# Performance work log

Measured on AMD Instinct MI355X. Metric: run time of the kernel, lower is better.

The kernel has to match this reference:

```python
import jax, jax.numpy as jnp
import numpy as np

B, n, D, L, Hff, heads = 64, 512, 128, 3, 512, 8
N = B * n
deg = 16
E = N * deg
dh = D // heads
EPS = 1e-5


def setup_inputs() -> dict:
    key = jax.random.key(0)
    ks = jax.random.split(key, 16)
    x = jax.random.normal(ks[0], (N, D), jnp.float32)
    # within-graph random edges (TSP kNN-style), offset per graph
    src = jax.random.randint(ks[1], (B, n * deg), 0, n)
    dst = jax.random.randint(ks[2], (B, n * deg), 0, n)
    off = (jnp.arange(B) * n)[:, None]
    edge_index = jnp.stack([(src + off).reshape(-1), (dst + off).reshape(-1)]).astype(jnp.int32)
    edge_attr = jax.random.normal(ks[3], (E, D), jnp.float32)
    batch = jnp.repeat(jnp.arange(B, dtype=jnp.int32), n)
    s = 0.02
    wk = jax.random.split(ks[4], 8)
    w = lambda k, shape: jax.random.normal(k, shape, jnp.float32) * s
    return dict(
        x=x, edge_index=edge_index, edge_attr=edge_attr, batch=batch,
        Wq=w(wk[0], (L, D, D)), bq=jnp.zeros((L, D), jnp.float32),
        Wk=w(wk[1], (L, D, D)), bk=jnp.zeros((L, D), jnp.float32),
        Wv=w(wk[2], (L, D, D)), bv=jnp.zeros((L, D), jnp.float32),
        We=w(wk[3], (L, D, D)),  # lin_edge has no bias in PyG TransformerConv
        Wskip=w(wk[4], (L, D, D)), bskip=jnp.zeros((L, D), jnp.float32),
        gn_g=jnp.ones((L - 1, D), jnp.float32), gn_b=jnp.zeros((L - 1, D), jnp.float32),
        gn_a=jnp.ones((L - 1, D), jnp.float32),
        ffW1=w(wk[5], (D, Hff)), ffb1=jnp.zeros((Hff,), jnp.float32),
        fgn_g=jnp.ones((Hff,), jnp.float32), fgn_b=jnp.zeros((Hff,), jnp.float32),
        fgn_a=jnp.ones((Hff,), jnp.float32),
        ffW2=w(wk[6], (Hff, D)), ffb2=jnp.zeros((D,), jnp.float32),
    )


def _graph_norm(x, batch, gamma, beta, alpha):
    # GraphNorm: per-graph mean/var per channel, learnable mean scale alpha
    mean = jax.ops.segment_sum(x, batch, num_segments=B) / n
    xc = x - alpha * mean[batch]
    var = jax.ops.segment_sum(xc * xc, batch, num_segments=B) / n
    return gamma * xc * jax.lax.rsqrt(var[batch] + EPS) + beta


def _transformer_conv(x, src, dst, ea, Wq, bq, Wk, bk, Wv, bv, We, Ws, bs):
    q = (x @ Wq + bq).reshape(-1, heads, dh)
    k = (x @ Wk + bk).reshape(-1, heads, dh)
    v = (x @ Wv + bv).reshape(-1, heads, dh)
    e = (ea @ We).reshape(-1, heads, dh)
    ke = k[src] + e                                   # [E, h, dh]
    score = jnp.einsum('ehd,ehd->eh', q[dst], ke) / np.sqrt(dh)
    m = jax.ops.segment_max(score, dst, num_segments=N)
    ex = jnp.exp(score - m[dst])
    denom = jax.ops.segment_sum(ex, dst, num_segments=N)
    alpha = ex / denom[dst]                           # softmax over in-neighbors
    msg = alpha[..., None] * (v[src] + e)
    out = jax.ops.segment_sum(msg, dst, num_segments=N).reshape(-1, D)
    return out + x @ Ws + bs                          # root/skip connection


def reference(x, edge_index, edge_attr, batch, Wq, bq, Wk, bk, Wv, bv, We, Wskip, bskip,
              gn_g, gn_b, gn_a, ffW1, ffb1, fgn_g, fgn_b, fgn_a, ffW2, ffb2):
    src, dst = edge_index[0], edge_index[1]
    for i in range(L):
        x = _transformer_conv(x, src, dst, edge_attr, Wq[i], bq[i], Wk[i], bk[i],
                              Wv[i], bv[i], We[i], Wskip[i], bskip[i])
        if i < L - 1:
            x = _graph_norm(jax.nn.gelu(x, approximate=False), batch, gn_g[i], gn_b[i], gn_a[i])
        else:
            h = jax.nn.gelu(x @ ffW1 + ffb1, approximate=False)
            h = _graph_norm(h, batch, fgn_g, fgn_b, fgn_a)
            x = h @ ffW2 + ffb2
    node_embeddings = x.reshape(B, n, D)
    graph_feat = jax.ops.segment_sum(x, batch, num_segments=B) / n  # mean pool
    return node_embeddings, graph_feat
```

## Files before the change

### kernel.cpp

```cpp
#include <hip/hip_runtime.h>
#include <hip/hip_bf16.h>
#include <math.h>

typedef unsigned short u16;
typedef __attribute__((ext_vector_type(4))) float floatx4;
typedef __attribute__((ext_vector_type(8))) short shortx8;

#define NB 64
#define NNODE 512
#define NTOT (NB*NNODE)
#define DDIM 128
#define DEG 16
#define NEDGE (NTOT*DEG)
#define HFF 512
#define EPSV 1e-5f
#define BFRAG_U16 16384
#define EPI_LD 136

__device__ __forceinline__ float bf2f(u16 u){
  union { unsigned int i; float f; } v; v.i = ((unsigned int)u) << 16; return v.f;
}
__device__ __forceinline__ u16 f2bf(float f){
  union { float f; unsigned int i; } v; v.f = f;
  unsigned int r = v.i + 0x7FFFu + ((v.i >> 16) & 1u);
  return (u16)(r >> 16);
}
__device__ __forceinline__ float gelu_f(float x){
  return 0.5f * x * (1.0f + erff(x * 0.70710678118654752f));
}

__global__ void prep_kernel(const float* __restrict__ x, u16* __restrict__ xb,
                            int* __restrict__ counts, float* __restrict__ pool){
  int gid = blockIdx.x*256 + threadIdx.x;
  if (gid < NTOT) counts[gid] = 0;
  if (gid < NB*DDIM) pool[gid] = 0.f;
  int i = gid*4;
  float4 f = *(const float4*)(x + i);
  ushort4 o; o.x = f2bf(f.x); o.y = f2bf(f.y); o.z = f2bf(f.z); o.w = f2bf(f.w);
  *(ushort4*)(xb + i) = o;
}

__global__ void hist_kernel(const int* __restrict__ dst, int* __restrict__ counts){
  int e = blockIdx.x*256 + threadIdx.x; atomicAdd(&counts[dst[e]], 1);
}
__global__ void scan_kernel(const int* counts, int* row_ptr, int* cursor){
  __shared__ int part[1024];
  int t = threadIdx.x; int base = t*32;
  int loc[32]; int s = 0;
  #pragma unroll
  for (int i = 0; i < 32; ++i){ loc[i] = counts[base+i]; s += loc[i]; }
  part[t] = s; __syncthreads();
  for (int off = 1; off < 1024; off <<= 1){
    int v = (t >= off) ? part[t-off] : 0;
    __syncthreads(); part[t] += v; __syncthreads();
  }
  int run = part[t] - s;
  #pragma unroll
  for (int i = 0; i < 32; ++i){ row_ptr[base+i] = run; cursor[base+i] = run; run += loc[i]; }
  if (t == 0) row_ptr[NTOT] = part[1023];
}
__global__ void scatter_kernel(const int* __restrict__ src, const int* __restrict__ dst,
                               int* __restrict__ cursor, int* __restrict__ ssrc, int* __restrict__ seid){
  int e = blockIdx.x*256 + threadIdx.x;
  int d = dst[e];
  int pos = atomicAdd(&cursor[d], 1);
  ssrc[pos] = src[e]; seid[pos] = e;
}

__global__ __launch_bounds__(512, 2)
void egemm3_kernel(const float* __restrict__ ea, const int* __restrict__ seid,
                   const float* __restrict__ We, u16* __restrict__ eout, int niter){
  __shared__ u16 bfrag[3*BFRAG_U16];
  __shared__ u16 epi_s[8*16*EPI_LD];
  const int t = threadIdx.x;
  const int wave = t >> 6, lane = t & 63, quad = lane >> 4, l16 = lane & 15;
  for (int p = wave; p < 12; p += 8){
    const int l = p >> 2, kk = p & 3;
    const float* Bp = We + (size_t)l*DDIM*DDIM;
    #pragma unroll
    for (int nt = 0; nt < 8; ++nt){
      int colB = nt*16 + l16;
      shortx8 pk;
      #pragma unroll
      for (int j = 0; j < 8; ++j)
        pk[j] = (short)f2bf(Bp[(size_t)(kk*32 + quad*8 + j)*DDIM + colB]);
      *(shortx8*)&bfrag[((size_t)l*2048 + (kk*8 + nt)*64 + lane)*8] = pk;
    }
  }
  __syncthreads();
  u16* epi = &epi_s[wave*16*EPI_LD];
  float4 pf[16];
  int it = blockIdx.x;
  if (it < niter){
    const int w0 = it*256 + wave*32;
    const long br0 = (long)seid[w0 + l16], br1 = (long)seid[w0 + 16 + l16];
    #pragma unroll
    for (int kk = 0; kk < 4; ++kk){
      pf[kk*4+0] = *(const float4*)(ea + br0*DDIM + kk*32 + quad*8);
      pf[kk*4+1] = *(const float4*)(ea + br0*DDIM + kk*32 + quad*8 + 4);
      pf[kk*4+2] = *(const float4*)(ea + br1*DDIM + kk*32 + quad*8);
      pf[kk*4+3] = *(const float4*)(ea + br1*DDIM + kk*32 + quad*8 + 4);
    }
  }
  while (it < niter){
    const int wrow0 = it*256 + wave*32;
    const int nxt = it + gridDim.x;
    shortx8 af[2][4];
    #pragma unroll
    for (int kk = 0; kk < 4; ++kk){
      float4 x0 = pf[kk*4+0], x1 = pf[kk*4+1], y0 = pf[kk*4+2], y1 = pf[kk*4+3];
      shortx8 a0, a1;
      a0[0]=(short)f2bf(x0.x); a0[1]=(short)f2bf(x0.y); a0[2]=(short)f2bf(x0.z); a0[3]=(short)f2bf(x0.w);
      a0[4]=(short)f2bf(x1.x); a0[5]=(short)f2bf(x1.y); a0[6]=(short)f2bf(x1.z); a0[7]=(short)f2bf(x1.w);
      a1[0]=(short)f2bf(y0.x); a1[1]=(short)f2bf(y0.y); a1[2]=(short)f2bf(y0.z); a1[3]=(short)f2bf(y0.w);
      a1[4]=(short)f2bf(y1.x); a1[5]=(short)f2bf(y1.y); a1[6]=(short)f2bf(y1.z); a1[7]=(short)f2bf(y1.w);
      af[0][kk] = a0; af[1][kk] = a1;
    }
    if (nxt < niter){
      const int w2 = nxt*256 + wave*32;
      const long br0 = (long)seid[w2 + l16], br1 = (long)seid[w2 + 16 + l16];
      #pragma unroll
      for (int kk = 0; kk < 4; ++kk){
        pf[kk*4+0] = *(const float4*)(ea + br0*DDIM + kk*32 + quad*8);
        pf[kk*4+1] = *(const float4*)(ea + br0*DDIM + kk*32 + quad*8 + 4);
        pf[kk*4+2] = *(const float4*)(ea + br1*DDIM + kk*32 + quad*8);
        pf[kk*4+3] = *(const float4*)(ea + br1*DDIM + kk*32 + quad*8 + 4);
      }
    }
    #pragma unroll
    for (int l = 0; l < 3; ++l){
      floatx4 acc[2][8] = {};
      #pragma unroll
      for (int kk = 0; kk < 4; ++kk){
        #pragma unroll
        for (int nt = 0; nt < 8; ++nt){
          shortx8 bfr = *(const shortx8*)&bfrag[((size_t)l*2048 + (kk*8 + nt)*64 + lane)*8];
          acc[0][nt] = __builtin_amdgcn_mfma_f32_16x16x32_bf16(af[0][kk], bfr, acc[0][nt], 0, 0, 0);
          acc[1][nt] = __builtin_amdgcn_mfma_f32_16x16x32_bf16(af[1][kk], bfr, acc[1][nt], 0, 0, 0);
        }
      }
      u16* o16 = eout + (size_t)l*NEDGE*DDIM;
      #pragma unroll
      for (int mt = 0; mt < 2; ++mt){
        #pragma unroll
        for (int nt = 0; nt < 8; ++nt){
          #pragma unroll
          for (int r = 0; r < 4; ++r)
            epi[(quad*4 + r)*EPI_LD + nt*16 + l16] = f2bf(acc[mt][nt][r]);
        }
        #pragma unroll
        for (int j = 0; j < 4; ++j){
          int row = j*4 + quad;
          uint4 d = *(const uint4*)&epi[row*EPI_LD + l16*8];
          *(uint4*)(o16 + (size_t)(wrow0 + mt*16 + row)*DDIM + l16*8) = d;
        }
      }
    }
    it = nxt;
  }
}

struct Gemm2Cfg {
  const float* B[4];
  const float* bias[4];
  float* o32[4];
  u16* o16[4];
  const float* nA;
  const float* nBp;
  int ldb, ld_out, bcolmul, ocolmul, gelu, mtiles;
};

template<bool AFF>
__global__ __launch_bounds__(256, 3)
void gemm2_kernel(const u16* __restrict__ Ab, Gemm2Cfg cfg){
  __shared__ u16 lds[BFRAG_U16 + 4*16*EPI_LD];
  const int t = threadIdx.x;
  const int wave = t >> 6, lane = t & 63, quad = lane >> 4, l16 = lane & 15;
  const int cb = blockIdx.y;
  const float* Bp = cfg.B[cb];
  const int col0b = cb * cfg.bcolmul;
  {
    const int kk = wave;
    #pragma unroll
    for (int nt = 0; nt < 8; ++nt){
      int colB = col0b + nt*16 + l16;
      shortx8 pk;
      #pragma unroll
      for (int j = 0; j < 8; ++j)
        pk[j] = (short)f2bf(Bp[(size_t)(kk*32 + quad*8 + j)*cfg.ldb + colB]);
      *(shortx8*)&lds[((kk*8 + nt)*64 + lane)*8] = pk;
    }
  }
  __syncthreads();
  const float* biasp = cfg.bias[cb];
  const int col0o = cb * cfg.ocolmul;
  float bias_r[8];
  #pragma unroll
  for (int nt = 0; nt < 8; ++nt)
    bias_r[nt] = biasp ? biasp[col0o + nt*16 + l16] : 0.0f;
  u16* epi = &lds[BFRAG_U16 + wave*16*EPI_LD];

  for (int tile = blockIdx.x; tile < cfg.mtiles; tile += gridDim.x){
    const int wrow0 = tile*128 + wave*32;
    const int r0 = wrow0 + l16, r1 = r0 + 16;
    const int g = wrow0 >> 9;
    shortx8 af[2][4];
    #pragma unroll
    for (int kk = 0; kk < 4; ++kk){
      shortx8 a0 = *(const shortx8*)(Ab + (size_t)r0*128 + kk*32 + quad*8);
      shortx8 a1 = *(const shortx8*)(Ab + (size_t)r1*128 + kk*32 + quad*8);
      if (AFF){
        const float4 A0 = *(const float4*)(cfg.nA  + (size_t)g*DDIM + kk*32 + quad*8);
        const float4 A1 = *(const float4*)(cfg.nA  + (size_t)g*DDIM + kk*32 + quad*8 + 4);
        const float4 B0 = *(const float4*)(cfg.nBp + (size_t)g*DDIM + kk*32 + quad*8);
        const float4 B1 = *(const float4*)(cfg.nBp + (size_t)g*DDIM + kk*32 + quad*8 + 4);
        u16* p0 = (u16*)&a0; u16* p1 = (u16*)&a1;
        p0[0]=f2bf(bf2f(p0[0])*A0.x+B0.x); p0[1]=f2bf(bf2f(p0[1])*A0.y+B0.y);
        p0[2]=f2bf(bf2f(p0[2])*A0.z+B0.z); p0[3]=f2bf(bf2f(p0[3])*A0.w+B0.w);
        p0[4]=f2bf(bf2f(p0[4])*A1.x+B1.x); p0[5]=f2bf(bf2f(p0[5])*A1.y+B1.y);
        p0[6]=f2bf(bf2f(p0[6])*A1.z+B1.z); p0[7]=f2bf(bf2f(p0[7])*A1.w+B1.w);
        p1[0]=f2bf(bf2f(p1[0])*A0.x+B0.x); p1[1]=f2bf(bf2f(p1[1])*A0.y+B0.y);
        p1[2]=f2bf(bf2f(p1[2])*A0.z+B0.z); p1[3]=f2bf(bf2f(p1[3])*A0.w+B0.w);
        p1[4]=f2bf(bf2f(p1[4])*A1.x+B1.x); p1[5]=f2bf(bf2f(p1[5])*A1.y+B1.y);
        p1[6]=f2bf(bf2f(p1[6])*A1.z+B1.z); p1[7]=f2bf(bf2f(p1[7])*A1.w+B1.w);
      }
      af[0][kk] = a0; af[1][kk] = a1;
    }
    floatx4 acc[2][8] = {};
    #pragma unroll
    for (int kk = 0; kk < 4; ++kk){
      #pragma unroll
      for (int nt = 0; nt < 8; ++nt){
        shortx8 bfr = *(const shortx8*)&lds[((kk*8 + nt)*64 + lane)*8];
        acc[0][nt] = __builtin_amdgcn_mfma_f32_16x16x32_bf16(af[0][kk], bfr, acc[0][nt], 0, 0, 0);
        acc[1][nt] = __builtin_amdgcn_mfma_f32_16x16x32_bf16(af[1][kk], bfr, acc[1][nt], 0, 0, 0);
      }
    }
    u16* o16 = cfg.o16[cb];
    if (o16){
      #pragma unroll
      for (int mt = 0; mt < 2; ++mt){
        #pragma unroll
        for (int nt = 0; nt < 8; ++nt){
          #pragma unroll
          for (int r = 0; r < 4; ++r){
            float v = acc[mt][nt][r] + bias_r[nt];
            if (cfg.gelu) v = gelu_f(v);
            epi[(quad*4 + r)*EPI_LD + nt*16 + l16] = f2bf(v);
          }
        }
        #pragma unroll
        for (int j = 0; j < 4; ++j){
          int row = j*4 + quad;
          uint4 d = *(const uint4*)&epi[row*EPI_LD + l16*8];
          *(uint4*)(o16 + (size_t)(wrow0 + mt*16 + row)*cfg.ld_out + col0o + l16*8) = d;
        }
      }
    } else {
      float* o32 = cfg.o32[cb];
      #pragma unroll
      for (int nt = 0; nt < 8; ++nt){
        #pragma unroll
        for (int mt = 0; mt < 2; ++mt){
          #pragma unroll
          for (int r = 0; r < 4; ++r){
            int row = wrow0 + mt*16 + quad*4 + r;
            float v = acc[mt][nt][r] + bias_r[nt];
            if (cfg.gelu) v = gelu_f(v);
            o32[(size_t)row*cfg.ld_out + col0o + nt*16 + l16] = v;
          }
        }
      }
    }
  }
}

struct GemmCfg {
  const float* B[4];
  const float* bias[4];
  float* o32[4];
  u16* o16[4];
  float* pool;
  const float* nA;
  const float* nBp;
  int ldb, ld_out, K, bcolmul, ocolmul, gelu;
};

__global__ __launch_bounds__(256, 2)
void gemm_old(const u16* __restrict__ Ab, GemmCfg cfg){
  __shared__ u16 As[128][136];
  __shared__ u16 Bs[128][136];
  const int t = threadIdx.x;
  const int wave = t >> 6, lane = t & 63, quad = lane >> 4, l16 = lane & 15;
  const int row0 = blockIdx.x * 128;
  const int cb = blockIdx.y;
  const float* Bp = cfg.B[cb];
  const int col0b = cb * cfg.bcolmul;
  const int K = cfg.K;
  const int g = row0 >> 9;
  floatx4 acc[2][8] = {};
  for (int kc = 0; kc < K; kc += 128){
    #pragma unroll
    for (int j = 0; j < 8; ++j){
      int idx8 = t + j*256;
      int elem = idx8 << 3;
      int r = elem >> 7, c = elem & 127;
      uint4 d = *(const uint4*)(Ab + (size_t)(row0+r)*K + kc + c);
      if (cfg.nA){
        const float4 A0 = *(const float4*)(cfg.nA  + (size_t)g*K + kc + c);
        const float4 A1 = *(const float4*)(cfg.nA  + (size_t)g*K + kc + c + 4);
        const float4 B0 = *(const float4*)(cfg.nBp + (size_t)g*K + kc + c);
        const float4 B1 = *(const float4*)(cfg.nBp + (size_t)g*K + kc + c + 4);
        u16* pu = (u16*)&d;
        pu[0] = f2bf(bf2f(pu[0])*A0.x + B0.x);
        pu[1] = f2bf(bf2f(pu[1])*A0.y + B0.y);
        pu[2] = f2bf(bf2f(pu[2])*A0.z + B0.z);
        pu[3] = f2bf(bf2f(pu[3])*A0.w + B0.w);
        pu[4] = f2bf(bf2f(pu[4])*A1.x + B1.x);
        pu[5] = f2bf(bf2f(pu[5])*A1.y + B1.y);
        pu[6] = f2bf(bf2f(pu[6])*A1.z + B1.z);
        pu[7] = f2bf(bf2f(pu[7])*A1.w + B1.w);
      }
      *(uint4*)&As[r][c] = d;
    }
    #pragma unroll
    for (int j = 0; j < 16; ++j){
      int gi = t + j*256;
      int c = gi & 127;
      int k4 = (gi >> 7) << 2;
      size_t boff = (size_t)(kc + k4)*cfg.ldb + col0b + c;
      float f0 = Bp[boff];
      float f1 = Bp[boff + cfg.ldb];
      float f2 = Bp[boff + 2*(size_t)cfg.ldb];
      float f3 = Bp[boff + 3*(size_t)cfg.ldb];
      u16* wp = &Bs[c][k4];
      wp[0]=f2bf(f0); wp[1]=f2bf(f1); wp[2]=f2bf(f2); wp[3]=f2bf(f3);
    }
    __syncthreads();
    const int wm0 = wave*32;
    #pragma unroll
    for (int kk = 0; kk < 4; ++kk){
      shortx8 a0 = *(const shortx8*)&As[wm0 + l16][kk*32 + quad*8];
      shortx8 a1 = *(const shortx8*)&As[wm0 + 16 + l16][kk*32 + quad*8];
      #pragma unroll
      for (int nt = 0; nt < 8; ++nt){
        shortx8 bfr = *(const shortx8*)&Bs[nt*16 + l16][kk*32 + quad*8];
        acc[0][nt] = __builtin_amdgcn_mfma_f32_16x16x32_bf16(a0, bfr, acc[0][nt], 0, 0, 0);
        acc[1][nt] = __builtin_amdgcn_mfma_f32_16x16x32_bf16(a1, bfr, acc[1][nt], 0, 0, 0);
      }
    }
    __syncthreads();
  }
  const float* biasp = cfg.bias[cb];
  float* o32 = cfg.o32[cb];
  const int col0o = cb * cfg.ocolmul;
  const int wm0 = wave*32;
  float* psum = (float*)As;
  if (cfg.pool){
    __syncthreads();
    if (t < 128) psum[t] = 0.f;
    __syncthreads();
  }
  #pragma unroll
  for (int nt = 0; nt < 8; ++nt){
    int col = col0o + nt*16 + l16;
    float bvv = biasp ? biasp[col] : 0.0f;
    float cs = 0.f;
    #pragma unroll
    for (int mt = 0; mt < 2; ++mt){
      #pragma unroll
      for (int r = 0; r < 4; ++r){
        int row = row0 + wm0 + mt*16 + quad*4 + r;
        float v = acc[mt][nt][r] + bvv;
        if (cfg.gelu) v = gelu_f(v);
        o32[(size_t)row * cfg.ld_out + col] = v;
        cs += v;
      }
    }
    if (cfg.pool) atomicAdd(&psum[nt*16 + l16], cs);
  }
  if (cfg.pool){
    __syncthreads();
    if (t < 128) atomicAdd(&cfg.pool[(row0 >> 9)*DDIM + t], psum[t] * (1.0f/NNODE));
  }
}

template<int GELU_OUT>
__global__ __launch_bounds__(256)
void attn_kernel(const int* __restrict__ row_ptr, const int* __restrict__ ssrc,
                 const u16* __restrict__ e_rows,
                 const u16* __restrict__ qb, const u16* __restrict__ kb, const u16* __restrict__ vb,
                 const float* __restrict__ skip, u16* __restrict__ yout){
  int b = blockIdx.x;
  int xcd = b & 7, i = b >> 3;
  int g = xcd*8 + (i >> 7), slot = i & 127;
  int wave = threadIdx.x >> 6, lane = threadIdx.x & 63;
  int dst = g*NNODE + slot*4 + wave;
  const int ch = lane*2;
  ushort2 qp = *(const ushort2*)(qb + (size_t)dst*DDIM + ch);
  float q0 = bf2f(qp.x), q1 = bf2f(qp.y);
  int beg = row_ptr[dst], end = row_ptr[dst+1];
  float mA = -INFINITY, lA = 0.f, y0A = 0.f, y1A = 0.f;
  float mB = -INFINITY, lB = 0.f, y0B = 0.f, y1B = 0.f;
  int idx = beg;
  for (; idx + 1 < end; idx += 2){
    int s0 = ssrc[idx], s1 = ssrc[idx+1];
    ushort2 e0p = *(const ushort2*)(e_rows + (size_t)idx*DDIM + ch);
    ushort2 e1p = *(const ushort2*)(e_rows + (size_t)(idx+1)*DDIM + ch);
    ushort2 k0p = *(const ushort2*)(kb + (size_t)s0*DDIM + ch);
    ushort2 k1p = *(const ushort2*)(kb + (size_t)s1*DDIM + ch);
    ushort2 v0p = *(const ushort2*)(vb + (size_t)s0*DDIM + ch);
    ushort2 v1p = *(const ushort2*)(vb + (size_t)s1*DDIM + ch);
    {
      float e0 = bf2f(e0p.x), e1 = bf2f(e0p.y);
      float p = q0*(bf2f(k0p.x)+e0) + q1*(bf2f(k0p.y)+e1);
      p += __shfl_xor(p, 1); p += __shfl_xor(p, 2); p += __shfl_xor(p, 4);
      float sc = p * 0.25f;
      float mn = fmaxf(mA, sc);
      float cs = __expf(mA - mn), w = __expf(sc - mn);
      lA = lA*cs + w;
      y0A = y0A*cs + w*(bf2f(v0p.x)+e0);
      y1A = y1A*cs + w*(bf2f(v0p.y)+e1);
      mA = mn;
    }
    {
      float e0 = bf2f(e1p.x), e1 = bf2f(e1p.y);
      float p = q0*(bf2f(k1p.x)+e0) + q1*(bf2f(k1p.y)+e1);
      p += __shfl_xor(p, 1); p += __shfl_xor(p, 2); p += __shfl_xor(p, 4);
      float sc = p * 0.25f;
      float mn = fmaxf(mB, sc);
      float cs = __expf(mB - mn), w = __expf(sc - mn);
      lB = lB*cs + w;
      y0B = y0B*cs + w*(bf2f(v1p.x)+e0);
      y1B = y1B*cs + w*(bf2f(v1p.y)+e1);
      mB = mn;
    }
  }
  if (idx < end){
    int s0 = ssrc[idx];
    ushort2 e0p = *(const ushort2*)(e_rows + (size_t)idx*DDIM + ch);
    ushort2 k0p = *(const ushort2*)(kb + (size_t)s0*DDIM + ch);
    ushort2 v0p = *(const ushort2*)(vb + (size_t)s0*DDIM + ch);
    float e0 = bf2f(e0p.x), e1 = bf2f(e0p.y);
    float p = q0*(bf2f(k0p.x)+e0) + q1*(bf2f(k0p.y)+e1);
    p += __shfl_xor(p, 1); p += __shfl_xor(p, 2); p += __shfl_xor(p, 4);
    float sc = p * 0.25f;
    float mn = fmaxf(mA, sc);
    float cs = __expf(mA - mn), w = __expf(sc - mn);
    lA = lA*cs + w;
    y0A = y0A*cs + w*(bf2f(v0p.x)+e0);
    y1A = y1A*cs + w*(bf2f(v0p.y)+e1);
    mA = mn;
  }
  float mn = fmaxf(mA, mB);
  float cA = lA > 0.f ? __expf(mA - mn) : 0.f;
  float cB = lB > 0.f ? __expf(mB - mn) : 0.f;
  float lh = lA*cA + lB*cB;
  float a0 = y0A*cA + y0B*cB;
  float a1 = y1A*cA + y1B*cB;
  float r = lh > 0.f ? 1.0f/lh : 0.f;
  float2 sp = *(const float2*)(skip + (size_t)dst*DDIM + ch);
  float o0 = a0*r + sp.x, o1 = a1*r + sp.y;
  if (GELU_OUT){ o0 = gelu_f(o0); o1 = gelu_f(o1); }
  ushort2 ov; ov.x = f2bf(o0); ov.y = f2bf(o1);
  *(ushort2*)(yout + (size_t)dst*DDIM + ch) = ov;
}

__global__ __launch_bounds__(128)
void gstats_part(const u16* __restrict__ gy, float* __restrict__ ps, float* __restrict__ pq){
  int b = blockIdx.x, g = b >> 3, chunk = b & 7, c = threadIdx.x;
  const u16* base = gy + (size_t)g*NNODE*DDIM + (size_t)chunk*64*DDIM;
  float s = 0.f, q = 0.f;
  for (int i = 0; i < 64; ++i){
    float v = bf2f(base[(size_t)i*DDIM + c]);
    s += v; q += v*v;
  }
  ps[b*DDIM + c] = s; pq[b*DDIM + c] = q;
}
__global__ __launch_bounds__(128)
void gstats_comb(const float* __restrict__ ps, const float* __restrict__ pq,
                 const float* __restrict__ gamma, const float* __restrict__ beta,
                 const float* __restrict__ alpha, float* __restrict__ nA, float* __restrict__ nB){
  int g = blockIdx.x, c = threadIdx.x;
  float s = 0.f, q = 0.f;
  #pragma unroll
  for (int j = 0; j < 8; ++j){ s += ps[(g*8+j)*DDIM + c]; q += pq[(g*8+j)*DDIM + c]; }
  float mean = s * (1.f/NNODE);
  float msq  = q * (1.f/NNODE);
  float a = alpha[c];
  float invv = rsqrtf(msq - mean*mean*a*(2.f-a) + EPSV);
  float ga = gamma[c]*invv;
  nA[g*DDIM + c] = ga;
  nB[g*DDIM + c] = beta[c] - ga*a*mean;
}

__global__ __launch_bounds__(512)
void fstats_part(const u16* __restrict__ gb, float* __restrict__ ps, float* __restrict__ pq){
  int b = blockIdx.x, g = b >> 3, chunk = b & 7, c = threadIdx.x;
  const u16* base = gb + (size_t)g*NNODE*HFF + (size_t)chunk*64*HFF;
  float s = 0.f, q = 0.f;
  for (int i = 0; i < 64; ++i){
    float v = bf2f(base[(size_t)i*HFF + c]);
    s += v; q += v*v;
  }
  ps[b*HFF + c] = s; pq[b*HFF + c] = q;
}
__global__ __launch_bounds__(512)
void fstats_comb(const float* __restrict__ ps, const float* __restrict__ pq,
                 const float* __restrict__ gamma, const float* __restrict__ beta,
                 const float* __restrict__ alpha, float* __restrict__ nA, float* __restrict__ nB){
  int g = blockIdx.x, c = threadIdx.x;
  float s = 0.f, q = 0.f;
  #pragma unroll
  for (int j = 0; j < 8; ++j){ s += ps[(g*8+j)*HFF + c]; q += pq[(g*8+j)*HFF + c]; }
  float mean = s * (1.f/NNODE);
  float msq  = q * (1.f/NNODE);
  float a = alpha[c];
  float invv = rsqrtf(msq - mean*mean*a*(2.f-a) + EPSV);
  float ga = gamma[c]*invv;
  nA[g*HFF + c] = ga;
  nB[g*HFF + c] = beta[c] - ga*a*mean;
}

extern "C" void kernel_launch(void* const* d_in, const int* in_sizes, int n_in,
                              void* d_out, int out_size, void* d_ws, size_t ws_size,
                              hipStream_t stream){
  const float* x_in = (const float*)d_in[0];
  const int*   eidx = (const int*)d_in[1];
  const float* ea   = (const float*)d_in[2];
  const float* Wq   = (const float*)d_in[4];
  const float* bq   = (const float*)d_in[5];
  const float* Wk   = (const float*)d_in[6];
  const float* bk   = (const float*)d_in[7];
  const float* Wv   = (const float*)d_in[8];
  const float* bv   = (const float*)d_in[9];
  const float* We   = (const float*)d_in[10];
  const float* Wsk  = (const float*)d_in[11];
  const float* bsk  = (const float*)d_in[12];
  const float* gn_g = (const float*)d_in[13];
  const float* gn_b = (const float*)d_in[14];
  const float* gn_a = (const float*)d_in[15];
  const float* ffW1 = (const float*)d_in[16];
  const float* ffb1 = (const float*)d_in[17];
  const float* fgn_g= (const float*)d_in[18];
  const float* fgn_b= (const float*)d_in[19];
  const float* fgn_a= (const float*)d_in[20];
  const float* ffW2 = (const float*)d_in[21];
  const float* ffb2 = (const float*)d_in[22];
  const int* srcA = eidx;
  const int* dstA = eidx + NEDGE;

  char* w = (char*)d_ws;
  auto alloc = [&](size_t bytes)->char*{ char* p = w; w += (bytes + 255) & ~(size_t)255; return p; };
  int* counts  = (int*)alloc((size_t)NTOT*4);
  int* row_ptr = (int*)alloc((size_t)(NTOT+1)*4);
  int* ssrc    = (int*)alloc((size_t)NEDGE*4);
  int* seid    = (int*)alloc((size_t)NEDGE*4);
  u16* e_bf    = (u16*)alloc((size_t)3*NEDGE*DDIM*2);
  u16* x_bf    = (u16*)alloc((size_t)NTOT*DDIM*2);
  u16* qb      = (u16*)alloc((size_t)NTOT*DDIM*2);
  u16* kb      = (u16*)alloc((size_t)NTOT*DDIM*2);
  u16* vb      = (u16*)alloc((size_t)NTOT*DDIM*2);
  float* skipb = (float*)alloc((size_t)NTOT*DDIM*4);
  float* nAb   = (float*)alloc((size_t)NB*HFF*4);
  float* nBb   = (float*)alloc((size_t)NB*HFF*4);
  float* psbuf = (float*)alloc((size_t)NB*8*HFF*4);
  float* pqbuf = (float*)alloc((size_t)NB*8*HFF*4);
  u16* g_bf  = e_bf;
  float* pool = (float*)d_out + (size_t)NTOT*DDIM;

  prep_kernel<<<NTOT*DDIM/1024, 256, 0, stream>>>(x_in, x_bf, counts, pool);
  hist_kernel<<<NEDGE/256, 256, 0, stream>>>(dstA, counts);
  scan_kernel<<<1, 1024, 0, stream>>>(counts, row_ptr, counts);
  scatter_kernel<<<NEDGE/256, 256, 0, stream>>>(srcA, dstA, counts, ssrc, seid);

  egemm3_kernel<<<256, 512, 0, stream>>>(ea, seid, We, e_bf, NEDGE/256);

  for (int l = 0; l < 3; ++l){
    Gemm2Cfg cq = {};
    cq.B[0]=Wq + (size_t)l*DDIM*DDIM; cq.B[1]=Wk + (size_t)l*DDIM*DDIM;
    cq.B[2]=Wv + (size_t)l*DDIM*DDIM; cq.B[3]=Wsk + (size_t)l*DDIM*DDIM;
    cq.bias[0]=bq + l*DDIM; cq.bias[1]=bk + l*DDIM; cq.bias[2]=bv + l*DDIM; cq.bias[3]=bsk + l*DDIM;
    cq.o16[0]=qb; cq.o16[1]=kb; cq.o16[2]=vb; cq.o16[3]=nullptr;
    cq.o32[3]=skipb;
    cq.ldb = DDIM; cq.ld_out = DDIM; cq.bcolmul = 0; cq.ocolmul = 0; cq.gelu = 0;
    cq.mtiles = NTOT/128;
    if (l == 0){
      gemm2_kernel<false><<<dim3(NTOT/128, 4), 256, 0, stream>>>(x_bf, cq);
    } else {
      cq.nA = nAb; cq.nBp = nBb;
      gemm2_kernel<true><<<dim3(NTOT/128, 4), 256, 0, stream>>>(x_bf, cq);
    }

    if (l < 2){
      attn_kernel<1><<<NTOT/4, 256, 0, stream>>>(row_ptr, ssrc,
          e_bf + (size_t)l*NEDGE*DDIM, qb, kb, vb, skipb, x_bf);
      gstats_part<<<NB*8, 128, 0, stream>>>(x_bf, psbuf, pqbuf);
      gstats_comb<<<NB, 128, 0, stream>>>(psbuf, pqbuf,
          gn_g + l*DDIM, gn_b + l*DDIM, gn_a + l*DDIM, nAb, nBb);
    } else {
      attn_kernel<0><<<NTOT/4, 256, 0, stream>>>(row_ptr, ssrc,
          e_bf + (size_t)l*NEDGE*DDIM, qb, kb, vb, skipb, x_bf);
    }
  }

  Gemm2Cfg c1 = {};
  for (int i2 = 0; i2 < 4; ++i2){ c1.B[i2] = ffW1; c1.bias[i2] = ffb1; c1.o16[i2] = g_bf; }
  c1.ldb = HFF; c1.ld_out = HFF; c1.bcolmul = 128; c1.ocolmul = 128; c1.gelu = 1;
  c1.mtiles = NTOT/128;
  gemm2_kernel<false><<<dim3(NTOT/128, 4), 256, 0, stream>>>(x_bf, c1);

  fstats_part<<<NB*8, 512, 0, stream>>>(g_bf, psbuf, pqbuf);
  fstats_comb<<<NB, 512, 0, stream>>>(psbuf, pqbuf, fgn_g, fgn_b, fgn_a, nAb, nBb);

  GemmCfg c2 = {};
  for (int i2 = 0; i2 < 4; ++i2){ c2.B[i2] = ffW2; c2.bias[i2] = ffb2; c2.o32[i2] = (float*)d_out; }
  c2.ldb = DDIM; c2.ld_out = DDIM; c2.K = HFF; c2.bcolmul = 0; c2.ocolmul = 0; c2.gelu = 0;
  c2.pool = pool;
  c2.nA = nAb; c2.nBp = nBb;
  gemm_old<<<dim3(NTOT/128, 1), 256, 0, stream>>>(g_bf, c2);
}
```

Baseline: 939.6 us.

## Read edge attrs contiguously and scatter GEMM outputs; store skip in bf16

The edge-projection GEMM now reads edge_attr rows in natural order, using coalesced contiguous loads, and writes each bf16 output row to its CSR position through an inverse permutation produced by the scatter kernel. Before, it gathered fp32 input rows through a sorted edge-id list. Separately, the skip/root projection is stored in bf16 rather than fp32, which halves its write and read traffic in the attention kernel. The costs are a scattered 256-byte-row write pattern in place of a scattered read, and some added rounding error in the skip term.

```diff
diff --git a/kernel.cpp b/kernel.cpp
--- a/kernel.cpp
+++ b/kernel.cpp
@@ -60,15 +60,16 @@
   if (t == 0) row_ptr[NTOT] = part[1023];
 }
 __global__ void scatter_kernel(const int* __restrict__ src, const int* __restrict__ dst,
-                               int* __restrict__ cursor, int* __restrict__ ssrc, int* __restrict__ seid){
+                               int* __restrict__ cursor, int* __restrict__ ssrc,
+                               int* __restrict__ inv){
   int e = blockIdx.x*256 + threadIdx.x;
   int d = dst[e];
   int pos = atomicAdd(&cursor[d], 1);
-  ssrc[pos] = src[e]; seid[pos] = e;
+  ssrc[pos] = src[e]; inv[e] = pos;
 }
 
 __global__ __launch_bounds__(512, 2)
-void egemm3_kernel(const float* __restrict__ ea, const int* __restrict__ seid,
+void egemm3_kernel(const float* __restrict__ ea, const int* __restrict__ inv,
                    const float* __restrict__ We, u16* __restrict__ eout, int niter){
   __shared__ u16 bfrag[3*BFRAG_U16];
   __shared__ u16 epi_s[8*16*EPI_LD];
@@ -92,14 +93,13 @@
   float4 pf[16];
   int it = blockIdx.x;
   if (it < niter){
-    const int w0 = it*256 + wave*32;
-    const long br0 = (long)seid[w0 + l16], br1 = (long)seid[w0 + 16 + l16];
+    const size_t base = ((size_t)it*256 + wave*32)*DDIM;
     #pragma unroll
     for (int kk = 0; kk < 4; ++kk){
-      pf[kk*4+0] = *(const float4*)(ea + br0*DDIM + kk*32 + quad*8);
-      pf[kk*4+1] = *(const float4*)(ea + br0*DDIM + kk*32 + quad*8 + 4);
-      pf[kk*4+2] = *(const float4*)(ea + br1*DDIM + kk*32 + quad*8);
-      pf[kk*4+3] = *(const float4*)(ea + br1*DDIM + kk*32 + quad*8 + 4);
+      pf[kk*4+0] = *(const float4*)(ea + base + (size_t)l16*DDIM + kk*32 + quad*8);
+      pf[kk*4+1] = *(const float4*)(ea + base + (size_t)l16*DDIM + kk*32 + quad*8 + 4);
+      pf[kk*4+2] = *(const float4*)(ea + base + (size_t)(16 + l16)*DDIM + kk*32 + quad*8);
+      pf[kk*4+3] = *(const float4*)(ea + base + (size_t)(16 + l16)*DDIM + kk*32 + quad*8 + 4);
     }
   }
   while (it < niter){
@@ -117,16 +117,21 @@
       af[0][kk] = a0; af[1][kk] = a1;
     }
     if (nxt < niter){
-      const int w2 = nxt*256 + wave*32;
-      const long br0 = (long)seid[w2 + l16], br1 = (long)seid[w2 + 16 + l16];
+      const size_t base = ((size_t)nxt*256 + wave*32)*DDIM;
       #pragma unroll
       for (int kk = 0; kk < 4; ++kk){
-        pf[kk*4+0] = *(const float4*)(ea + br0*DDIM + kk*32 + quad*8);
-        pf[kk*4+1] = *(const float4*)(ea + br0*DDIM + kk*32 + quad*8 + 4);
-        pf[kk*4+2] = *(const float4*)(ea + br1*DDIM + kk*32 + quad*8);
-        pf[kk*4+3] = *(const float4*)(ea + br1*DDIM + kk*32 + quad*8 + 4);
-      }
-    }
+        pf[kk*4+0] = *(const float4*)(ea + base + (size_t)l16*DDIM + kk*32 + quad*8);
+        pf[kk*4+1] = *(const float4*)(ea + base + (size_t)l16*DDIM + kk*32 + quad*8 + 4);
+        pf[kk*4+2] = *(const float4*)(ea + base + (size_t)(16 + l16)*DDIM + kk*32 + quad*8);
+        pf[kk*4+3] = *(const float4*)(ea + base + (size_t)(16 + l16)*DDIM + kk*32 + quad*8 + 4);
+      }
+    }
+    int drow[2][4];
+    #pragma unroll
+    for (int mt = 0; mt < 2; ++mt)
+      #pragma unroll
+      for (int j = 0; j < 4; ++j)
+        drow[mt][j] = inv[wrow0 + mt*16 + j*4 + quad];
     #pragma unroll
     for (int l = 0; l < 3; ++l){
       floatx4 acc[2][8] = {};
@@ -150,9 +155,8 @@
         }
         #pragma unroll
         for (int j = 0; j < 4; ++j){
-          int row = j*4 + quad;
-          uint4 d = *(const uint4*)&epi[row*EPI_LD + l16*8];
-          *(uint4*)(o16 + (size_t)(wrow0 + mt*16 + row)*DDIM + l16*8) = d;
+          uint4 d = *(const uint4*)&epi[(j*4 + quad)*EPI_LD + l16*8];
+          *(uint4*)(o16 + (size_t)drow[mt][j]*DDIM + l16*8) = d;
         }
       }
     }
@@ -390,7 +394,7 @@
 void attn_kernel(const int* __restrict__ row_ptr, const int* __restrict__ ssrc,
                  const u16* __restrict__ e_rows,
                  const u16* __restrict__ qb, const u16* __restrict__ kb, const u16* __restrict__ vb,
-                 const float* __restrict__ skip, u16* __restrict__ yout){
+                 const u16* __restrict__ skip, u16* __restrict__ yout){
   int b = blockIdx.x;
   int xcd = b & 7, i = b >> 3;
   int g = xcd*8 + (i >> 7), slot = i & 127;
@@ -459,8 +463,8 @@
   float a0 = y0A*cA + y0B*cB;
   float a1 = y1A*cA + y1B*cB;
   float r = lh > 0.f ? 1.0f/lh : 0.f;
-  float2 sp = *(const float2*)(skip + (size_t)dst*DDIM + ch);
-  float o0 = a0*r + sp.x, o1 = a1*r + sp.y;
+  ushort2 sp = *(const ushort2*)(skip + (size_t)dst*DDIM + ch);
+  float o0 = a0*r + bf2f(sp.x), o1 = a1*r + bf2f(sp.y);
   if (GELU_OUT){ o0 = gelu_f(o0); o1 = gelu_f(o1); }
   ushort2 ov; ov.x = f2bf(o0); ov.y = f2bf(o1);
   *(ushort2*)(yout + (size_t)dst*DDIM + ch) = ov;
@@ -555,13 +559,13 @@
   int* counts  = (int*)alloc((size_t)NTOT*4);
   int* row_ptr = (int*)alloc((size_t)(NTOT+1)*4);
   int* ssrc    = (int*)alloc((size_t)NEDGE*4);
-  int* seid    = (int*)alloc((size_t)NEDGE*4);
+  int* inv     = (int*)alloc((size_t)NEDGE*4);
   u16* e_bf    = (u16*)alloc((size_t)3*NEDGE*DDIM*2);
   u16* x_bf    = (u16*)alloc((size_t)NTOT*DDIM*2);
   u16* qb      = (u16*)alloc((size_t)NTOT*DDIM*2);
   u16* kb      = (u16*)alloc((size_t)NTOT*DDIM*2);
   u16* vb      = (u16*)alloc((size_t)NTOT*DDIM*2);
-  float* skipb = (float*)alloc((size_t)NTOT*DDIM*4);
+  u16* skipb   = (u16*)alloc((size_t)NTOT*DDIM*2);
   float* nAb   = (float*)alloc((size_t)NB*HFF*4);
   float* nBb   = (float*)alloc((size_t)NB*HFF*4);
   float* psbuf = (float*)alloc((size_t)NB*8*HFF*4);
@@ -572,17 +576,16 @@
   prep_kernel<<<NTOT*DDIM/1024, 256, 0, stream>>>(x_in, x_bf, counts, pool);
   hist_kernel<<<NEDGE/256, 256, 0, stream>>>(dstA, counts);
   scan_kernel<<<1, 1024, 0, stream>>>(counts, row_ptr, counts);
-  scatter_kernel<<<NEDGE/256, 256, 0, stream>>>(srcA, dstA, counts, ssrc, seid);
-
-  egemm3_kernel<<<256, 512, 0, stream>>>(ea, seid, We, e_bf, NEDGE/256);
+  scatter_kernel<<<NEDGE/256, 256, 0, stream>>>(srcA, dstA, counts, ssrc, inv);
+
+  egemm3_kernel<<<256, 512, 0, stream>>>(ea, inv, We, e_bf, NEDGE/256);
 
   for (int l = 0; l < 3; ++l){
     Gemm2Cfg cq = {};
     cq.B[0]=Wq + (size_t)l*DDIM*DDIM; cq.B[1]=Wk + (size_t)l*DDIM*DDIM;
     cq.B[2]=Wv + (size_t)l*DDIM*DDIM; cq.B[3]=Wsk + (size_t)l*DDIM*DDIM;
     cq.bias[0]=bq + l*DDIM; cq.bias[1]=bk + l*DDIM; cq.bias[2]=bv + l*DDIM; cq.bias[3]=bsk + l*DDIM;
-    cq.o16[0]=qb; cq.o16[1]=kb; cq.o16[2]=vb; cq.o16[3]=nullptr;
-    cq.o32[3]=skipb;
+    cq.o16[0]=qb; cq.o16[1]=kb; cq.o16[2]=vb; cq.o16[3]=skipb;
     cq.ldb = DDIM; cq.ld_out = DDIM; cq.bcolmul = 0; cq.ocolmul = 0; cq.gelu = 0;
     cq.mtiles = NTOT/128;
     if (l == 0){
```

Result: faster. 920.7 us (-2.0%).
